# Optimization experiments

Hardware: AMD Instinct MI355X
Metric: run time of the kernel (lower is better)

Reference implementation:

```python
import jax, jax.numpy as jnp
import numpy as np

EMB = 32      # emb_size = input_size // 2
IN = 64       # input_size
H = 128       # hidden_size
OUT = 256     # output_size (byte vocab)
TEMP = 1e-3   # Decoder_lstm.temperature


def _bytes(x):
    # x: [N] nonneg int32 -> [N, 4] big-endian bytes (vectorized get_bytes_2d)
    shifts = jnp.array([24, 16, 8, 0], dtype=x.dtype)
    return (x[:, None] >> shifts) & 0xFF


def _embed4(tables, byts):
    # tables: [4, 256, EMB]; byts: [N, 4] -> [N, 4*EMB] (concat of 4 gathers)
    return jnp.concatenate([tables[i][byts[:, i]] for i in range(4)], axis=-1)


def _encoder(x, W, b):
    # Encoder: sigmoid(Linear(4*EMB -> EMB))
    return jax.nn.sigmoid(x @ W.T + b)


def _lstm(xs, h0, c0, W_ih, W_hh, b_ih, b_hh):
    # xs: [S, B, IN]; PyTorch gate order i, f, g, o
    def step(carry, x_t):
        h, c = carry
        g = x_t @ W_ih.T + b_ih + h @ W_hh.T + b_hh  # [B, 4H]
        i, f, gg, o = jnp.split(g, 4, axis=-1)
        c = jax.nn.sigmoid(f) * c + jax.nn.sigmoid(i) * jnp.tanh(gg)
        h = jax.nn.sigmoid(o) * jnp.tanh(c)
        return (h, c), None
    (hf, cf), _ = jax.lax.scan(step, (h0, c0), xs)
    return hf, cf


def reference(inp, h0, c0, pc_emb, addr_emb, enc_W, enc_b, W_ih, W_hh, b_ih, b_hh, dec_W, dec_b, fc1_W, fc1_b, fc2_W, fc2_b):
    b, s, _ = inp.shape
    pc = inp[:, :, 0].reshape(-1)
    ad = inp[:, :, 1].reshape(-1)
    # byte decomposition + embedding gather + TimeDistributed encoder MLP
    pc_e = _encoder(_embed4(pc_emb, _bytes(pc)), enc_W, enc_b).reshape(b, s, EMB)
    ad_e = _encoder(_embed4(addr_emb, _bytes(ad)), enc_W, enc_b).reshape(b, s, EMB)
    emb = jnp.concatenate([pc_e, ad_e], axis=-1)  # [b, s, IN]
    # deterministic surrogate for KDE sample mean (expected value of 200 KDE draws)
    dist = jnp.mean(emb, axis=1)  # [b, IN]
    hf, _ = _lstm(jnp.swapaxes(emb, 0, 1), h0[0], c0[0], W_ih, W_hh, b_ih, b_hh)
    h_n = hf[None]  # [1, b, H] == hidden_cell[0]
    # Decoder_lstm: 4 parallel linears + low-temperature softmax
    logits = jnp.einsum('xbh,koh->kxbo', h_n, dec_W) + dec_b[:, None, None, :]  # [4,1,b,OUT]
    probs = jax.nn.softmax(logits / TEMP, axis=-1)
    # get_freq_rec: probs @ embedding tables, encoder MLP, concat dist, small MLP
    be = jnp.einsum('kxbo,koe->xbke', probs, addr_emb).reshape(1, b, 4 * EMB)
    fe = _encoder(be, enc_W, enc_b)[0]  # [b, EMB]
    fr_in = jnp.concatenate([fe, dist], axis=-1)  # [b, 3*EMB]
    fr = jax.nn.sigmoid(jax.nn.relu(fr_in @ fc1_W.T + fc1_b) @ fc2_W.T + fc2_b)
    return probs, logits, fr[:, 0], fr[:, 1]


def setup_inputs() -> dict:
    ks = jax.random.split(jax.random.key(0), 18)
    B, S = 64, 2048
    g = lambda k, shp: 0.1 * jax.random.normal(k, shp, dtype=jnp.float32)
    return {
        'inp': jax.random.randint(ks[0], (B, S, 2), 0, 2147483647, dtype=jnp.int32),
        'h0': g(ks[1], (1, B, H)),
        'c0': g(ks[2], (1, B, H)),
        'pc_emb': g(ks[3], (4, 256, EMB)),
        'addr_emb': g(ks[4], (4, 256, EMB)),
        'enc_W': g(ks[5], (EMB, 4 * EMB)),
        'enc_b': g(ks[6], (EMB,)),
        'W_ih': g(ks[7], (4 * H, IN)),
        'W_hh': g(ks[8], (4 * H, H)),
        'b_ih': g(ks[9], (4 * H,)),
        'b_hh': g(ks[10], (4 * H,)),
        'dec_W': g(ks[11], (4, OUT, H)),
        'dec_b': g(ks[12], (4, OUT)),
        'fc1_W': g(ks[13], (10, 3 * EMB)),
        'fc1_b': g(ks[14], (10,)),
        'fc2_W': g(ks[15], (2, 10)),
        'fc2_b': g(ks[16], (2,)),
    }
```

## Files before the change

kernel.cpp:

```cpp
#include <hip/hip_runtime.h>
#include <math.h>
#include <stdint.h>

#define EMBS 32
#define INS 64
#define HS 128
#define OUTS 256
#define BS 64
#define SS 2048

typedef _Float16 half2v __attribute__((ext_vector_type(2)));
typedef _Float16 half8  __attribute__((ext_vector_type(8)));
typedef float f32x4 __attribute__((ext_vector_type(4)));
typedef unsigned int uint2v __attribute__((ext_vector_type(2)));

typedef union { half8 v; half2v p[4]; } h8u;

static constexpr size_t WS_DIST  = (size_t)BS * SS * INS;
static constexpr size_t WS_HFIN  = WS_DIST + (size_t)BS * INS;
static constexpr size_t WS_P     = WS_HFIN + (size_t)BS * HS;
static constexpr size_t WS_XW    = WS_P + 2ull * 4 * 256 * 32;
static constexpr size_t WS_SMALL = WS_XW;
static constexpr size_t WS_BIG   = WS_XW + (size_t)BS * SS * 256;

__device__ __forceinline__ float fexp2(float x) {
#if __has_builtin(__builtin_amdgcn_exp2f)
    return __builtin_amdgcn_exp2f(x);
#else
    return exp2f(x);
#endif
}
__device__ __forceinline__ float frcp(float x) {
#if __has_builtin(__builtin_amdgcn_rcpf)
    return __builtin_amdgcn_rcpf(x);
#else
    return 1.f / x;
#endif
}
__device__ __forceinline__ float sigm(float x)  { return frcp(1.f + fexp2(-1.44269504f * x)); }
__device__ __forceinline__ float ftanh(float x) { return 1.f - 2.f * frcp(1.f + fexp2(2.88539008f * x)); }

__device__ __forceinline__ float fdot2f(half2v a, half2v b, float c) {
#if __has_builtin(__builtin_amdgcn_fdot2)
    return __builtin_amdgcn_fdot2(a, b, c, false);
#else
    return c + (float)a.x * (float)b.x + (float)a.y * (float)b.y;
#endif
}

__device__ __forceinline__ half2v pack2(float a, float b) {
    half2v r; r.x = (_Float16)a; r.y = (_Float16)b; return r;
}

__device__ __forceinline__ float pswap32(float x, bool lo) {
#if __has_builtin(__builtin_amdgcn_permlane32_swap)
    uint2v r = __builtin_amdgcn_permlane32_swap(
        __builtin_bit_cast(unsigned, x), __builtin_bit_cast(unsigned, x),
        false, false);
    return __builtin_bit_cast(float, lo ? r.y : r.x);
#else
    return __shfl_xor(x, 32, 64);
#endif
}

__device__ __forceinline__ void gate_map(int tid, int& u, bool& lo, int& g0, int& g1) {
    int l = tid & 63;
    u = ((tid >> 6) << 5) + (l & 31);
    lo = (l < 32);
    g0 = lo ? u : 128 + u;
    g1 = lo ? 256 + u : 384 + u;
}

__global__ __launch_bounds__(256) void k_pre(
    const float* __restrict__ pc_emb, const float* __restrict__ ad_emb,
    const float* __restrict__ encW, const float* __restrict__ encB,
    float* __restrict__ P)
{
    int idx = blockIdx.x * 256 + threadIdx.x;
    int e = idx & 31, by = (idx >> 5) & 255, i = (idx >> 13) & 3, st = idx >> 15;
    const float* tbl = (st ? ad_emb : pc_emb) + ((size_t)i * 256 + by) * EMBS;
    const float* w = encW + e * 128 + i * 32;
    float acc = (i == 0) ? encB[e] : 0.f;
    #pragma unroll
    for (int k = 0; k < 32; k++) acc += w[k] * tbl[k];
    P[idx] = acc;
}

__global__ __launch_bounds__(256) void k_embed2(
    const int* __restrict__ inp, const float* __restrict__ P,
    float* __restrict__ emb)
{
    int idx = blockIdx.x * 256 + threadIdx.x;
    size_t base = (size_t)idx;
    int2 pa = ((const int2*)inp)[base];
    float* outp = emb + base * INS;

    #pragma unroll
    for (int st = 0; st < 2; st++) {
        int v = st ? pa.y : pa.x;
        const float* Ps = P + st * 32768;
        float acc[32];
        #pragma unroll
        for (int i = 0; i < 4; i++) {
            int by = (v >> (24 - 8 * i)) & 255;
            const float4* row = (const float4*)(Ps + ((size_t)i * 256 + by) * 32);
            #pragma unroll
            for (int k = 0; k < 8; k++) {
                float4 f = row[k];
                if (i == 0) {
                    acc[k * 4 + 0] = f.x; acc[k * 4 + 1] = f.y;
                    acc[k * 4 + 2] = f.z; acc[k * 4 + 3] = f.w;
                } else {
                    acc[k * 4 + 0] += f.x; acc[k * 4 + 1] += f.y;
                    acc[k * 4 + 2] += f.z; acc[k * 4 + 3] += f.w;
                }
            }
        }
        #pragma unroll
        for (int e = 0; e < 32; e++) outp[st * 32 + e] = sigm(acc[e]);
    }
}

__global__ __launch_bounds__(256) void k_dist(const float* __restrict__ emb,
                                              float* __restrict__ dist)
{
    int b = blockIdx.x;
    int j = threadIdx.x & 63;
    int grp = threadIdx.x >> 6;
    float s = 0.f;
    for (int t = grp; t < SS; t += 4) s += emb[((size_t)b * SS + t) * INS + j];
    __shared__ float red[4][64];
    red[grp][j] = s;
    __syncthreads();
    if (grp == 0)
        dist[b * 64 + j] = (red[0][j] + red[1][j] + red[2][j] + red[3][j]) * (1.f / SS);
}

#define XW_ROWS 64
__global__ __launch_bounds__(256) void k_xw(
    const float* __restrict__ emb, const float* __restrict__ Wih,
    const float* __restrict__ bih, const float* __restrict__ bhh,
    half2v* __restrict__ xwv)
{
    int tid = threadIdx.x;
    size_t r0 = (size_t)blockIdx.x * XW_ROWS;
    int u, g0, g1; bool lo;
    gate_map(tid, u, lo, g0, g1);

    half2v wa[32], wb[32];
    const float* pa_ = Wih + (size_t)g0 * INS;
    const float* pb_ = Wih + (size_t)g1 * INS;
    #pragma unroll
    for (int i = 0; i < 32; i++) {
        wa[i] = pack2(pa_[2 * i], pa_[2 * i + 1]);
        wb[i] = pack2(pb_[2 * i], pb_[2 * i + 1]);
    }
    float ba = bih[g0] + bhh[g0], bb = bih[g1] + bhh[g1];

    __shared__ alignas(16) half2v xsh[XW_ROWS * 32];
    const float4* src = (const float4*)(emb + r0 * INS);
    #pragma unroll
    for (int k = 0; k < 4; k++) {
        int fi = k * 256 + tid;
        float4 v = src[fi];
        xsh[fi * 2]     = pack2(v.x, v.y);
        xsh[fi * 2 + 1] = pack2(v.z, v.w);
    }
    __syncthreads();

    #pragma unroll 2
    for (int r = 0; r < XW_ROWS; r++) {
        const half8* xr8 = (const half8*)&xsh[r * 32];
        h8u x8[8];
        #pragma unroll
        for (int k = 0; k < 8; k++) x8[k].v = xr8[k];
        float a0 = 0.f, a1 = 0.f, b0 = 0.f, b1 = 0.f;
        #pragma unroll
        for (int i = 0; i < 32; i += 2) {
            half2v x0 = x8[i >> 2].p[i & 3], x1 = x8[(i + 1) >> 2].p[(i + 1) & 3];
            a0 = fdot2f(x0, wa[i], a0);
            a1 = fdot2f(x1, wa[i + 1], a1);
            b0 = fdot2f(x0, wb[i], b0);
            b1 = fdot2f(x1, wb[i + 1], b1);
        }
        xwv[(r0 + r) * 256 + tid] = pack2(ba + a0 + a1, bb + b0 + b1);
    }
}

__global__ __launch_bounds__(256, 1) void k_lstm9(
    const half2v* __restrict__ xw, const float* __restrict__ h0,
    const float* __restrict__ c0, const float* __restrict__ Whh,
    float* __restrict__ hfin)
{
    int b = blockIdx.x;
    int tid = threadIdx.x;
    int u, g0_, g1_; bool lo;
    gate_map(tid, u, lo, g0_, g1_);
    int koff = lo ? 0 : 64;

    half2v wI[32], wF[32], wG[32], wO[32];
    {
        const float* rI = Whh + (size_t)(u)       * HS + koff;
        const float* rF = Whh + (size_t)(128 + u) * HS + koff;
        const float* rG = Whh + (size_t)(256 + u) * HS + koff;
        const float* rO = Whh + (size_t)(384 + u) * HS + koff;
        #pragma unroll
        for (int i = 0; i < 32; i++) {
            wI[i] = pack2(rI[2 * i], rI[2 * i + 1]);
            wF[i] = pack2(rF[2 * i], rF[2 * i + 1]);
            wG[i] = pack2(rG[2 * i], rG[2 * i + 1]);
            wO[i] = pack2(rO[2 * i], rO[2 * i + 1]);
        }
    }

    __shared__ alignas(16) _Float16 hsh[2][HS];
    float c = 0.f, h = 0.f;
    if (!lo) c = c0[b * HS + u];
    if (tid < 128) hsh[0][tid] = (_Float16)h0[b * HS + tid];
    __syncthreads();

    const half2v* xwrow = xw + (size_t)b * SS * 256 + tid;
    half2v xb0 = xwrow[0];
    half2v xb1 = xwrow[256];
    half2v xb2 = xwrow[512];
    half2v xb3 = xwrow[768];

#define LSTEP(XB, RB, TN)                                                      \
    {                                                                          \
        const half8* hb8 = (const half8*)(&hsh[RB][0] + koff);                 \
        h8u h8[8];                                                             \
        _Pragma("unroll")                                                      \
        for (int k_ = 0; k_ < 8; k_++) h8[k_].v = hb8[k_];        \
        float pIa = 0.f, pFa = 0.f, pGa = 0.f, pOa = 0.f;                      \
        float pIb = 0.f, pFb = 0.f, pGb = 0.f, pOb = 0.f;                      \
        _Pragma("unroll")                                                      \
        for (int j_ = 0; j_ < 16; j_++) {                                      \
            half2v hv = h8[j_ >> 2].p[j_ & 3];                                 \
            pIa = fdot2f(hv, wI[j_], pIa);                                     \
            pFa = fdot2f(hv, wF[j_], pFa);                                     \
            pGa = fdot2f(hv, wG[j_], pGa);                                     \
            pOa = fdot2f(hv, wO[j_], pOa);                                     \
        }                                                                      \
        _Pragma("unroll")                                                      \
        for (int j_ = 16; j_ < 32; j_++) {                                     \
            half2v hv = h8[j_ >> 2].p[j_ & 3];                                 \
            pIb = fdot2f(hv, wI[j_], pIb);                                     \
            pFb = fdot2f(hv, wF[j_], pFb);                                     \
            pGb = fdot2f(hv, wG[j_], pGb);                                     \
            pOb = fdot2f(hv, wO[j_], pOb);                                     \
        }                                                                      \
        float pI = pIa + pIb, pF = pFa + pFb;                                  \
        float pG = pGa + pGb, pO = pOa + pOb;                                  \
        float r1 = pswap32(lo ? pF : pI, lo);       \
        float r2 = pswap32(lo ? pO : pG, lo);       \
        float pre0 = (lo ? pI : pF) + r1 + (float)XB.x;                        \
        float pre1 = (lo ? pG : pO) + r2 + (float)XB.y;                        \
        float act0 = sigm(pre0);                            \
        float act1 = lo ? ftanh(pre1) : sigm(pre1);         \
        float pig = pswap32(act0 * act1, lo);             \
        if (!lo) {                                                             \
            c = __builtin_fmaf(act0, c, pig);                                  \
            h = act1 * ftanh(c);                                               \
            hsh[RB ^ 1][u] = (_Float16)h;                                      \
        }                                                                      \
        {                                                                      \
            int tn_ = (TN) < SS ? (TN) : (SS - 1);                             \
            XB = xwrow[(size_t)tn_ * 256];                                     \
        }                                                                      \
        asm volatile("s_waitcnt lgkmcnt(0)" ::: "memory");                     \
        __builtin_amdgcn_s_barrier();                                          \
        __builtin_amdgcn_sched_barrier(0);                                     \
    }

    for (int t = 0; t < SS; t += 4) {
        LSTEP(xb0, 0, t + 4)
        LSTEP(xb1, 1, t + 5)
        LSTEP(xb2, 0, t + 6)
        LSTEP(xb3, 1, t + 7)
    }
#undef LSTEP

    if (!lo) hfin[b * HS + u] = h;
}

__global__ __launch_bounds__(256, 1) void k_lstm_fb(
    const float* __restrict__ emb, const float* __restrict__ h0,
    const float* __restrict__ c0, const float* __restrict__ Wih,
    const float* __restrict__ Whh, const float* __restrict__ bih,
    const float* __restrict__ bhh, float* __restrict__ hfin)
{
    int b = blockIdx.x;
    int tid = threadIdx.x;

    half2v wih[2][32], whh[2][64];
    #pragma unroll
    for (int g = 0; g < 2; g++) {
        int gg = tid + g * 256;
        const float* wr = Wih + (size_t)gg * INS;
        #pragma unroll
        for (int i = 0; i < 32; i++) wih[g][i] = pack2(wr[2 * i], wr[2 * i + 1]);
        const float* hr = Whh + (size_t)gg * HS;
        #pragma unroll
        for (int i = 0; i < 64; i++) whh[g][i] = pack2(hr[2 * i], hr[2 * i + 1]);
    }
    float bias0 = bih[tid] + bhh[tid];
    float bias1 = bih[tid + 256] + bhh[tid + 256];

    __shared__ alignas(16) half2v xh[96];
    __shared__ float f_act[128], o_act[128];
    __shared__ float xf[64], hf[128];

    float c = 0.f, h = 0.f;
    if (tid < 128) c = c0[b * HS + tid];

    const float* xrow = emb + (size_t)b * SS * INS;
    if (tid < 64) xf[tid] = xrow[tid];
    if (tid < 128) hf[tid] = h0[b * HS + tid];
    __syncthreads();
    if (tid < 32) xh[tid] = pack2(xf[2 * tid], xf[2 * tid + 1]);
    else if (tid < 96) { int uu = tid - 32; xh[tid] = pack2(hf[2 * uu], hf[2 * uu + 1]); }
    __syncthreads();

    for (int t = 0; t < SS; t++) {
        float xn = 0.f;
        if (tid >= 128 && tid < 192 && t + 1 < SS) xn = xrow[(size_t)(t + 1) * INS + (tid - 128)];

        float a0a = 0.f, a0b = 0.f, a1a = 0.f, a1b = 0.f;
        #pragma unroll
        for (int i = 0; i < 32; i += 2) {
            half2v x0 = xh[i], x1 = xh[i + 1];
            a0a = fdot2f(x0, wih[0][i], a0a);
            a0b = fdot2f(x1, wih[0][i + 1], a0b);
            a1a = fdot2f(x0, wih[1][i], a1a);
            a1b = fdot2f(x1, wih[1][i + 1], a1b);
        }
        #pragma unroll
        for (int i = 0; i < 64; i += 2) {
            half2v h0v = xh[32 + i], h1v = xh[32 + i + 1];
            a0a = fdot2f(h0v, whh[0][i], a0a);
            a0b = fdot2f(h1v, whh[0][i + 1], a0b);
            a1a = fdot2f(h0v, whh[1][i], a1a);
            a1b = fdot2f(h1v, whh[1][i + 1], a1b);
        }
        float a0 = bias0 + a0a + a0b;
        float a1 = bias1 + a1a + a1b;

        float iact = 0.f, gact = 0.f;
        if (tid < 128) { iact = sigm(a0); gact = ftanh(a1); }
        else           { f_act[tid - 128] = sigm(a0); o_act[tid - 128] = sigm(a1); }
        __syncthreads();

        if (tid < 128) {
            c = f_act[tid] * c + iact * gact;
            h = o_act[tid] * ftanh(c);
            hf[tid] = h;
        } else if (tid < 192) {
            xf[tid - 128] = xn;
        }
        __syncthreads();

        if (tid < 32) xh[tid] = pack2(xf[2 * tid], xf[2 * tid + 1]);
        else if (tid < 96) { int uu = tid - 32; xh[tid] = pack2(hf[2 * uu], hf[2 * uu + 1]); }
        __syncthreads();
    }
    if (tid < 128) hfin[b * HS + tid] = h;
}

__global__ __launch_bounds__(256) void k_head(
    const float* __restrict__ hfin, const float* __restrict__ decW,
    const float* __restrict__ decB, const float* __restrict__ ad_emb,
    const float* __restrict__ encW, const float* __restrict__ encB,
    const float* __restrict__ dist, const float* __restrict__ fc1W,
    const float* __restrict__ fc1b, const float* __restrict__ fc2W,
    const float* __restrict__ fc2b, float* __restrict__ outp)
{
    int b = blockIdx.x;
    int tid = threadIdx.x;
    __shared__ alignas(16) float hsh[128];
    __shared__ float logit_s[4][256];
    __shared__ float probs_s[4][256];
    __shared__ float be_s[128];
    __shared__ float fe_dist[96];
    __shared__ float fr1[10];

    if (tid < 128) hsh[tid] = hfin[b * HS + tid];
    __syncthreads();

    {
        f32x4 hv[32];
        const f32x4* h4 = (const f32x4*)hsh;
        #pragma unroll
        for (int j = 0; j < 32; j++) hv[j] = h4[j];
        #pragma unroll
        for (int k = 0; k < 4; k++) {
            const float4* w4 = (const float4*)(decW + ((size_t)k * OUTS + tid) * HS);
            float a0 = decB[k * OUTS + tid], a1 = 0.f;
            #pragma unroll
            for (int j = 0; j < 32; j++) {
                float4 wv = w4[j];
                a0 = __builtin_fmaf(hv[j][0], wv.x, a0);
                a1 = __builtin_fmaf(hv[j][1], wv.y, a1);
                a0 = __builtin_fmaf(hv[j][2], wv.z, a0);
                a1 = __builtin_fmaf(hv[j][3], wv.w, a1);
            }
            float acc = a0 + a1;
            logit_s[k][tid] = acc;
            outp[65536 + k * 16384 + b * 256 + tid] = acc;
        }
    }
    __syncthreads();

    {
        int k = tid >> 6, lane = tid & 63;
        float v0 = logit_s[k][lane],       v1 = logit_s[k][lane + 64];
        float v2 = logit_s[k][lane + 128], v3 = logit_s[k][lane + 192];
        float m = fmaxf(fmaxf(v0, v1), fmaxf(v2, v3));
        for (int off = 32; off; off >>= 1) m = fmaxf(m, __shfl_xor(m, off, 64));
        float e0 = fexp2((v0 - m) * 1442.695041f), e1 = fexp2((v1 - m) * 1442.695041f);
        float e2 = fexp2((v2 - m) * 1442.695041f), e3 = fexp2((v3 - m) * 1442.695041f);
        float s = e0 + e1 + e2 + e3;
        for (int off = 32; off; off >>= 1) s += __shfl_xor(s, off, 64);
        float inv = 1.f / s;
        float p0 = e0 * inv, p1 = e1 * inv, p2 = e2 * inv, p3 = e3 * inv;
        probs_s[k][lane] = p0;        probs_s[k][lane + 64] = p1;
        probs_s[k][lane + 128] = p2;  probs_s[k][lane + 192] = p3;
        outp[k * 16384 + b * 256 + lane] = p0;
        outp[k * 16384 + b * 256 + lane + 64] = p1;
        outp[k * 16384 + b * 256 + lane + 128] = p2;
        outp[k * 16384 + b * 256 + lane + 192] = p3;
    }
    __syncthreads();

    if (tid < 128) {
        int k = tid >> 5, e = tid & 31;
        const float* te = ad_emb + (size_t)k * OUTS * EMBS + e;
        float acc = 0.f;
        #pragma unroll 8
        for (int o = 0; o < OUTS; o++) acc += probs_s[k][o] * te[o * EMBS];
        be_s[tid] = acc;
    }
    __syncthreads();

    if (tid < 32) {
        const float* w = encW + tid * 128;
        float acc = encB[tid];
        #pragma unroll 8
        for (int kk = 0; kk < 128; kk++) acc += be_s[kk] * w[kk];
        fe_dist[tid] = sigm(acc);
    } else if (tid < 96) {
        fe_dist[tid] = dist[b * 64 + (tid - 32)];
    }
    __syncthreads();

    if (tid < 10) {
        float acc = fc1b[tid];
        for (int kk = 0; kk < 96; kk++) acc += fe_dist[kk] * fc1W[tid * 96 + kk];
        fr1[tid] = fmaxf(acc, 0.f);
    }
    __syncthreads();

    if (tid < 2) {
        float acc = fc2b[tid];
        for (int kk = 0; kk < 10; kk++) acc += fr1[kk] * fc2W[tid * 10 + kk];
        outp[131072 + tid * 64 + b] = sigm(acc);
    }
}

extern "C" void kernel_launch(void* const* d_in, const int* in_sizes, int n_in,
                              void* d_out, int out_size, void* d_ws, size_t ws_size,
                              hipStream_t stream)
{
    const int*   inp    = (const int*)d_in[0];
    const float* h0     = (const float*)d_in[1];
    const float* c0     = (const float*)d_in[2];
    const float* pc_emb = (const float*)d_in[3];
    const float* ad_emb = (const float*)d_in[4];
    const float* encW   = (const float*)d_in[5];
    const float* encB   = (const float*)d_in[6];
    const float* Wih    = (const float*)d_in[7];
    const float* Whh    = (const float*)d_in[8];
    const float* bih    = (const float*)d_in[9];
    const float* bhh    = (const float*)d_in[10];
    const float* decW   = (const float*)d_in[11];
    const float* decB   = (const float*)d_in[12];
    const float* fc1W   = (const float*)d_in[13];
    const float* fc1b   = (const float*)d_in[14];
    const float* fc2W   = (const float*)d_in[15];
    const float* fc2b   = (const float*)d_in[16];

    if (ws_size < WS_SMALL * 4ull) return;

    float* ws   = (float*)d_ws;
    float* emb  = ws;
    float* dist = ws + WS_DIST;
    float* hfin = ws + WS_HFIN;
    float* P    = ws + WS_P;
    float* outp = (float*)d_out;
    bool big = (ws_size >= WS_BIG * 4ull);

    hipLaunchKernelGGL(k_pre, dim3(256), dim3(256), 0, stream,
                       pc_emb, ad_emb, encW, encB, P);
    hipLaunchKernelGGL(k_embed2, dim3(512), dim3(256), 0, stream,
                       inp, P, emb);
    hipLaunchKernelGGL(k_dist, dim3(64), dim3(256), 0, stream, emb, dist);
    if (big) {
        half2v* xwv = (half2v*)(ws + WS_XW);
        hipLaunchKernelGGL(k_xw, dim3(BS * SS / XW_ROWS), dim3(256), 0, stream,
                           emb, Wih, bih, bhh, xwv);
        hipLaunchKernelGGL(k_lstm9, dim3(64), dim3(256), 0, stream,
                           xwv, h0, c0, Whh, hfin);
    } else {
        hipLaunchKernelGGL(k_lstm_fb, dim3(64), dim3(256), 0, stream,
                           emb, h0, c0, Wih, Whh, bih, bhh, hfin);
    }
    hipLaunchKernelGGL(k_head, dim3(64), dim3(256), 0, stream,
                       hfin, decW, decB, ad_emb, encW, encB, dist,
                       fc1W, fc1b, fc2W, fc2b, outp);
}
```

Measured before the change: 1.272 ms.

## Split LSTM recurrence across 512 threads with two gates per thread

The recurrent LSTM kernel now runs 512 threads per batch row instead of 256. Each thread holds weights for two gate rows over half of K rather than four, so the per-step dot-product chain on the serial critical path is halved. Partial sums are combined with a lane swap, and gate activations go through a unified sigmoid/tanh formula selected by per-thread constants. In exchange, each step now needs more cross-lane shuffles and a barrier spanning eight waves instead of four, and the xw loads use a remapped index.

```diff
diff --git a/kernel.cpp b/kernel.cpp
--- a/kernel.cpp
+++ b/kernel.cpp
@@ -187,39 +187,44 @@
     }
 }
 
-__global__ __launch_bounds__(256, 1) void k_lstm9(
+__global__ __launch_bounds__(512, 2) void k_lstm12(
     const half2v* __restrict__ xw, const float* __restrict__ h0,
     const float* __restrict__ c0, const float* __restrict__ Whh,
     float* __restrict__ hfin)
 {
     int b = blockIdx.x;
     int tid = threadIdx.x;
-    int u, g0_, g1_; bool lo;
-    gate_map(tid, u, lo, g0_, g1_);
-    int koff = lo ? 0 : 64;
-
-    half2v wI[32], wF[32], wG[32], wO[32];
+    int w = tid >> 6, l = tid & 63;
+    int u = (w << 4) + (l & 15);
+    int gp = (l >> 4) & 1;
+    int ks = l >> 5;
+    bool hi = (gp == 1);
+    bool lo32 = (l < 32);
+    int koff = ks * 64;
+
+    half2v wA[32], wB[32];
     {
-        const float* rI = Whh + (size_t)(u)       * HS + koff;
-        const float* rF = Whh + (size_t)(128 + u) * HS + koff;
-        const float* rG = Whh + (size_t)(256 + u) * HS + koff;
-        const float* rO = Whh + (size_t)(384 + u) * HS + koff;
+        const float* rA = Whh + (size_t)(gp * 128 + u) * HS + koff;
+        const float* rB = Whh + (size_t)(256 + gp * 128 + u) * HS + koff;
         #pragma unroll
         for (int i = 0; i < 32; i++) {
-            wI[i] = pack2(rI[2 * i], rI[2 * i + 1]);
-            wF[i] = pack2(rF[2 * i], rF[2 * i + 1]);
-            wG[i] = pack2(rG[2 * i], rG[2 * i + 1]);
-            wO[i] = pack2(rO[2 * i], rO[2 * i + 1]);
-        }
-    }
+            wA[i] = pack2(rA[2 * i], rA[2 * i + 1]);
+            wB[i] = pack2(rB[2 * i], rB[2 * i + 1]);
+        }
+    }
+
+    float zm  = hi ? -1.44269504f : 2.88539008f;
+    float sc  = hi ? 1.f : -2.f;
+    float off = hi ? 0.f : 1.f;
 
     __shared__ alignas(16) _Float16 hsh[2][HS];
     float c = 0.f, h = 0.f;
-    if (!lo) c = c0[b * HS + u];
+    if (hi) c = c0[b * HS + u];
     if (tid < 128) hsh[0][tid] = (_Float16)h0[b * HS + tid];
     __syncthreads();
 
-    const half2v* xwrow = xw + (size_t)b * SS * 256 + tid;
+    int xwi = ((u >> 5) << 6) + (gp << 5) + (u & 31);
+    const half2v* xwrow = xw + (size_t)b * SS * 256 + xwi;
     half2v xb0 = xwrow[0];
     half2v xb1 = xwrow[256];
     half2v xb2 = xwrow[512];
@@ -228,40 +233,35 @@
 #define LSTEP(XB, RB, TN)                                                      \
     {                                                                          \
         const half8* hb8 = (const half8*)(&hsh[RB][0] + koff);                 \
-        h8u h8[8];                                                             \
+        h8u h8v[8];                                                            \
         _Pragma("unroll")                                                      \
-        for (int k_ = 0; k_ < 8; k_++) h8[k_].v = hb8[k_];        \
-        float pIa = 0.f, pFa = 0.f, pGa = 0.f, pOa = 0.f;                      \
-        float pIb = 0.f, pFb = 0.f, pGb = 0.f, pOb = 0.f;                      \
+        for (int k_ = 0; k_ < 8; k_++) h8v[k_].v = hb8[k_];       \
+        float pA0 = 0.f, pA1 = 0.f, pB0 = 0.f, pB1 = 0.f;                      \
         _Pragma("unroll")                                                      \
         for (int j_ = 0; j_ < 16; j_++) {                                      \
-            half2v hv = h8[j_ >> 2].p[j_ & 3];                                 \
-            pIa = fdot2f(hv, wI[j_], pIa);                                     \
-            pFa = fdot2f(hv, wF[j_], pFa);                                     \
-            pGa = fdot2f(hv, wG[j_], pGa);                                     \
-            pOa = fdot2f(hv, wO[j_], pOa);                                     \
+            half2v hv = h8v[j_ >> 2].p[j_ & 3];                                \
+            pA0 = fdot2f(hv, wA[j_], pA0);                                     \
+            pB0 = fdot2f(hv, wB[j_], pB0);                                     \
         }                                                                      \
         _Pragma("unroll")                                                      \
         for (int j_ = 16; j_ < 32; j_++) {                                     \
-            half2v hv = h8[j_ >> 2].p[j_ & 3];                                 \
-            pIb = fdot2f(hv, wI[j_], pIb);                                     \
-            pFb = fdot2f(hv, wF[j_], pFb);                                     \
-            pGb = fdot2f(hv, wG[j_], pGb);                                     \
-            pOb = fdot2f(hv, wO[j_], pOb);                                     \
+            half2v hv = h8v[j_ >> 2].p[j_ & 3];                                \
+            pA1 = fdot2f(hv, wA[j_], pA1);                                     \
+            pB1 = fdot2f(hv, wB[j_], pB1);                                     \
         }                                                                      \
-        float pI = pIa + pIb, pF = pFa + pFb;                                  \
-        float pG = pGa + pGb, pO = pOa + pOb;                                  \
-        float r1 = pswap32(lo ? pF : pI, lo);       \
-        float r2 = pswap32(lo ? pO : pG, lo);       \
-        float pre0 = (lo ? pI : pF) + r1 + (float)XB.x;                        \
-        float pre1 = (lo ? pG : pO) + r2 + (float)XB.y;                        \
-        float act0 = sigm(pre0);                            \
-        float act1 = lo ? ftanh(pre1) : sigm(pre1);         \
-        float pig = pswap32(act0 * act1, lo);             \
-        if (!lo) {                                                             \
+        float pA = pA0 + pA1, pB = pB0 + pB1;                                  \
+                           \
+        float preA = pA + pswap32(pA, lo32) + (float)XB.x;                     \
+        float preB = pB + pswap32(pB, lo32) + (float)XB.y;                     \
+        float act0 = sigm(preA);                          \
+        float y = frcp(1.f + fexp2(zm * preB));                                \
+        float act1 = __builtin_fmaf(sc, y, off);          \
+                             \
+        float pig = __shfl_xor(act0 * act1, 16, 64);                           \
+        if (hi) {                                                              \
             c = __builtin_fmaf(act0, c, pig);                                  \
             h = act1 * ftanh(c);                                               \
-            hsh[RB ^ 1][u] = (_Float16)h;                                      \
+            if (ks == 0) hsh[RB ^ 1][u] = (_Float16)h;                         \
         }                                                                      \
         {                                                                      \
             int tn_ = (TN) < SS ? (TN) : (SS - 1);                             \
@@ -280,7 +280,7 @@
     }
 #undef LSTEP
 
-    if (!lo) hfin[b * HS + u] = h;
+    if (hi && ks == 0) hfin[b * HS + u] = h;
 }
 
 __global__ __launch_bounds__(256, 1) void k_lstm_fb(
@@ -507,7 +507,7 @@
         half2v* xwv = (half2v*)(ws + WS_XW);
         hipLaunchKernelGGL(k_xw, dim3(BS * SS / XW_ROWS), dim3(256), 0, stream,
                            emb, Wih, bih, bhh, xwv);
-        hipLaunchKernelGGL(k_lstm9, dim3(64), dim3(256), 0, stream,
+        hipLaunchKernelGGL(k_lstm12, dim3(64), dim3(512), 0, stream,
                            xwv, h0, c0, Whh, hfin);
     } else {
         hipLaunchKernelGGL(k_lstm_fb, dim3(64), dim3(256), 0, stream,
```

Result: slower. 1.476 ms (+16.0%).
